# Kernel tuning notes

Measured on AMD Instinct MI355X. Metric: run time of the kernel, lower is better.

Reference implementation:

```python
import jax, jax.numpy as jnp
import numpy as np

MAX_ITERS = 256  # matches init_kwargs max_iters


def setup_inputs() -> dict:
    key = jax.random.key(0)
    k1, k2 = jax.random.split(key)
    H = W = 4096
    # classic Mandelbrot viewing window
    c_real = jax.random.uniform(k1, (H, W), jnp.float32, -2.0, 0.5)
    c_imag = jax.random.uniform(k2, (H, W), jnp.float32, -1.25, 1.25)
    return {"c_real": c_real, "c_imag": c_imag}


def reference(c_real, c_imag):
    # z starts at c (NOT zero), as in the torch module
    zr0 = c_real
    zi0 = c_imag
    active0 = jnp.ones(c_real.shape, dtype=bool)
    counts0 = jnp.full(c_real.shape, float(MAX_ITERS), dtype=c_real.dtype)

    def body(step, state):
        zr, zi, active, counts = state
        escaped_now = active & (zr * zr + zi * zi >= 4.0)
        counts = jnp.where(escaped_now, step.astype(counts.dtype), counts)
        active = active & ~escaped_now
        # torch loop only updates z for step < max_iters
        do_update = active & (step < MAX_ITERS)
        next_real = zr * zr - zi * zi + c_real
        next_imag = 2.0 * zr * zi + c_imag
        zr = jnp.where(do_update, next_real, zr)
        zi = jnp.where(do_update, next_imag, zi)
        return (zr, zi, active, counts)

    _, _, _, counts = jax.lax.fori_loop(
        0, MAX_ITERS + 1, body, (zr0, zi0, active0, counts0)
    )
    return counts
```

## Files before the change

### kernel.cpp

```cpp
#include <hip/hip_runtime.h>


#define MAX_ITERS 256

__device__ __forceinline__ float mul32(float a, float b) {
    float d; asm("v_mul_f32 %0, %1, %2" : "=v"(d) : "v"(a), "v"(b)); return d;
}
__device__ __forceinline__ float add32(float a, float b) {
    float d; asm("v_add_f32 %0, %1, %2" : "=v"(d) : "v"(a), "v"(b)); return d;
}
__device__ __forceinline__ float fma32(float a, float b, float c) {
    float d; asm("v_fma_f32 %0, %1, %2, %3" : "=v"(d) : "v"(a), "v"(b), "v"(c)); return d;
}
__device__ __forceinline__ float fma32_negc(float a, float b, float c) {
    float d; asm("v_fma_f32 %0, %1, %2, -%3" : "=v"(d) : "v"(a), "v"(b), "v"(c)); return d;
}

__device__ __forceinline__ void iter_checks(float cr, float ci,
                                            float& zr, float& zi,
                                            float& act, float& cnt, int nchecks)
{
    #pragma unroll 8
    for (int s = 0; s < nchecks; ++s) {
        const float zi2 = mul32(zi, zi);
        const float mag = fma32(zr, zr, zi2);
        act = (mag < 4.0f) ? act : 0.0f;
        cnt = cnt + act;
        const float t   = fma32_negc(zr, zr, zi2);
        const float nr  = add32(t, cr);
        const float t2  = add32(zr, zr);
        zi = fma32(t2, zi, ci);
        zr = nr;
    }
}

__global__ void zero_ctrs(unsigned char* ws) {
    if (threadIdx.x < 64) *(unsigned*)(ws + (size_t)threadIdx.x * 64u) = 0u;
}

__global__ __launch_bounds__(256) void mandel_stage_a(
    const float* __restrict__ c_real, const float* __restrict__ c_imag,
    float* __restrict__ out, unsigned char* __restrict__ ws,
    unsigned seg_cap, int n)
{
    int i = blockIdx.x * blockDim.x + threadIdx.x;
    if (i >= n) return;
    const float cr = c_real[i];
    const float ci = c_imag[i];

    const float xq = cr - 0.25f;
    const float q  = xq * xq + ci * ci;
    const bool in_card = (q * (q + xq) - 0.25f * ci * ci) < -1e-3f;
    const float xb = cr + 1.0f;
    const bool in_bulb = (xb * xb + ci * ci) < (0.0625f - 1e-3f);
    const bool shortcut = in_card | in_bulb;

    float zr = cr, zi = ci, act = 1.0f, cnt = 0.0f;
    iter_checks(cr, ci, zr, zi, act, cnt, 16);

    const bool surv = (!shortcut) && (act != 0.0f);

    const unsigned long long m = __ballot(surv);
    if (m != 0ull) {
        const int lane = __builtin_amdgcn_mbcnt_hi(
            ~0u, __builtin_amdgcn_mbcnt_lo(~0u, 0));
        const int leader = (int)__ffsll((unsigned long long)m) - 1;
        const int seg = blockIdx.x & 63;
        unsigned* ctr = (unsigned*)(ws + (size_t)seg * 64u);
        unsigned base = 0u;
        if (lane == leader) base = atomicAdd(ctr, (unsigned)__popcll(m));
        base = (unsigned)__shfl((int)base, leader, 64);
        if (surv) {
            const unsigned rank = (unsigned)__popcll(m & ((1ull << lane) - 1ull));
            const unsigned slot = base + rank;
            if (slot < seg_cap) {
                float4* q1 = (float4*)(ws + 4096);
                int*    q2 = (int*)(ws + 4096 + (size_t)seg_cap * 64u * 16u);
                const size_t p = (size_t)seg * seg_cap + slot;
                q1[p] = make_float4(zr, zi, cr, ci);
                q2[p] = i;
                return;
            }
            iter_checks(cr, ci, zr, zi, act, cnt, 240);
            out[i] = cnt;
            return;
        }
    }
    out[i] = shortcut ? 256.0f : cnt;
}

__global__ __launch_bounds__(256) void mandel_stage_b(
    float* __restrict__ out, const unsigned char* __restrict__ ws,
    unsigned seg_cap, int blocks_per_seg)
{
    const int seg = (int)(blockIdx.x & 63u);
    const int grp = (int)(blockIdx.x >> 6);
    const unsigned cnt_s = *(const unsigned*)(ws + (size_t)seg * 64u);
    const unsigned nq = (cnt_s < seg_cap) ? cnt_s : seg_cap;
    const float4* q1 = (const float4*)(ws + 4096);
    const int*    q2 = (const int*)(ws + 4096 + (size_t)seg_cap * 64u * 16u);
    const unsigned stride = (unsigned)blocks_per_seg * 256u;
    for (unsigned j = (unsigned)grp * 256u + threadIdx.x; j < nq; j += stride) {
        const size_t p = (size_t)seg * seg_cap + j;
        const float4 rec = q1[p];
        const int idx = q2[p];
        float zr = rec.x, zi = rec.y;
        const float cr = rec.z, ci = rec.w;
        float act = 1.0f, cnt = 16.0f;
        iter_checks(cr, ci, zr, zi, act, cnt, 240);
        out[idx] = cnt;
    }
}

__global__ __launch_bounds__(256) void mandel_mono(
    const float* __restrict__ c_real, const float* __restrict__ c_imag,
    float* __restrict__ out, int n)
{
    int i = blockIdx.x * blockDim.x + threadIdx.x;
    if (i >= n) return;
    const float cr = c_real[i], ci = c_imag[i];
    float zr = cr, zi = ci, act = 1.0f, cnt = 0.0f;
    iter_checks(cr, ci, zr, zi, act, cnt, MAX_ITERS);
    out[i] = cnt;
}

extern "C" void kernel_launch(void* const* d_in, const int* in_sizes, int n_in,
                              void* d_out, int out_size, void* d_ws, size_t ws_size,
                              hipStream_t stream)
{
    const float* c_real = (const float*)d_in[0];
    const float* c_imag = (const float*)d_in[1];
    float* out = (float*)d_out;
    const int n = in_sizes[0];
    const int block = 256;
    const int gridA = (n + block - 1) / block;

    unsigned char* ws = (unsigned char*)d_ws;
    const size_t avail = (ws_size > 4096) ? (ws_size - 4096) : 0;
    unsigned seg_cap = (unsigned)(avail / (64u * 20u));

    if (seg_cap < 1024u) {
        mandel_mono<<<gridA, block, 0, stream>>>(c_real, c_imag, out, n);
        return;
    }

    zero_ctrs<<<1, 64, 0, stream>>>(ws);
    mandel_stage_a<<<gridA, block, 0, stream>>>(c_real, c_imag, out, ws,
                                                seg_cap, n);
    const int blocks_per_seg = 256;
    mandel_stage_b<<<64 * blocks_per_seg, block, 0, stream>>>(out, ws, seg_cap,
                                                              blocks_per_seg);
}
```

Measured before the change: 258.3 us.

## Process four points per thread with packed FP32 math in both stages

Each thread in both the filter and tail stages now iterates four Mandelbrot points at once, using v_pk_mul/fma/add_f32 inline asm so two points share each packed instruction. Stage A uses vectorized float4 loads and one atomic per wave covering all four ballots. Stage B splits each segment's queue into four strided quarters per thread and drops to 32 blocks per segment. This trades more registers and lower occupancy, plus intra-thread divergence where one of the four points runs all 240 iterations, for half the ALU instruction count.

```diff
diff --git a/kernel.cpp b/kernel.cpp
--- a/kernel.cpp
+++ b/kernel.cpp
@@ -2,6 +2,9 @@
 
 
 #define MAX_ITERS 256
+
+typedef __attribute__((ext_vector_type(2))) float f32x2;
+typedef __attribute__((ext_vector_type(4))) float f32x4;
 
 __device__ __forceinline__ float mul32(float a, float b) {
     float d; asm("v_mul_f32 %0, %1, %2" : "=v"(d) : "v"(a), "v"(b)); return d;
@@ -34,62 +37,148 @@
     }
 }
 
-__global__ void zero_ctrs(unsigned char* ws) {
-    if (threadIdx.x < 64) *(unsigned*)(ws + (size_t)threadIdx.x * 64u) = 0u;
-}
-
-__global__ __launch_bounds__(256) void mandel_stage_a(
-    const float* __restrict__ c_real, const float* __restrict__ c_imag,
-    float* __restrict__ out, unsigned char* __restrict__ ws,
-    unsigned seg_cap, int n)
-{
-    int i = blockIdx.x * blockDim.x + threadIdx.x;
-    if (i >= n) return;
-    const float cr = c_real[i];
-    const float ci = c_imag[i];
-
+__device__ __forceinline__ void zstep2(const f32x2 cr, const f32x2 ci,
+                                       f32x2& zr, f32x2& zi, f32x2& mag)
+{
+    f32x2 s, t, u;
+    asm("v_pk_mul_f32 %0, %5, %5\n\t"
+        "v_pk_fma_f32 %1, %4, %4, %0\n\t"
+        "v_pk_fma_f32 %2, %4, %4, %0 neg_lo:[0,0,1] neg_hi:[0,0,1]\n\t"
+        "v_pk_add_f32 %3, %4, %4\n\t"
+        "v_pk_add_f32 %4, %2, %6\n\t"
+        "v_pk_fma_f32 %5, %3, %5, %7"
+        : "=&v"(s), "=&v"(mag), "=&v"(t), "=&v"(u), "+v"(zr), "+v"(zi)
+        : "v"(cr), "v"(ci));
+}
+
+__device__ __forceinline__ void check4(
+    const f32x2 crA, const f32x2 ciA, f32x2& zrA, f32x2& ziA,
+    const f32x2 crB, const f32x2 ciB, f32x2& zrB, f32x2& ziB,
+    float& act0, float& act1, float& act2, float& act3,
+    float& cnt0, float& cnt1, float& cnt2, float& cnt3)
+{
+    f32x2 magA, magB;
+    zstep2(crA, ciA, zrA, ziA, magA);
+    zstep2(crB, ciB, zrB, ziB, magB);
+    act0 = (magA.x < 4.0f) ? act0 : 0.0f;  cnt0 += act0;
+    act1 = (magA.y < 4.0f) ? act1 : 0.0f;  cnt1 += act1;
+    act2 = (magB.x < 4.0f) ? act2 : 0.0f;  cnt2 += act2;
+    act3 = (magB.y < 4.0f) ? act3 : 0.0f;  cnt3 += act3;
+}
+
+__device__ __forceinline__ int lane_id() {
+    return __builtin_amdgcn_mbcnt_hi(~0u, __builtin_amdgcn_mbcnt_lo(~0u, 0));
+}
+
+__device__ __forceinline__ bool in_shortcut(float cr, float ci) {
     const float xq = cr - 0.25f;
     const float q  = xq * xq + ci * ci;
     const bool in_card = (q * (q + xq) - 0.25f * ci * ci) < -1e-3f;
     const float xb = cr + 1.0f;
     const bool in_bulb = (xb * xb + ci * ci) < (0.0625f - 1e-3f);
-    const bool shortcut = in_card | in_bulb;
-
-    float zr = cr, zi = ci, act = 1.0f, cnt = 0.0f;
-    iter_checks(cr, ci, zr, zi, act, cnt, 16);
-
-    const bool surv = (!shortcut) && (act != 0.0f);
-
-    const unsigned long long m = __ballot(surv);
-    if (m != 0ull) {
-        const int lane = __builtin_amdgcn_mbcnt_hi(
-            ~0u, __builtin_amdgcn_mbcnt_lo(~0u, 0));
-        const int leader = (int)__ffsll((unsigned long long)m) - 1;
+    return in_card | in_bulb;
+}
+
+__global__ void zero_ctrs(unsigned char* ws) {
+    if (threadIdx.x < 64)
+        *(unsigned*)(ws + (size_t)threadIdx.x * 64u) = 0u;
+}
+
+__global__ __launch_bounds__(256) void mandel_stage_a_q(
+    const float* __restrict__ c_real, const float* __restrict__ c_imag,
+    float* __restrict__ out, unsigned char* __restrict__ ws,
+    unsigned seg_cap, int n)
+{
+    const int tq = blockIdx.x * blockDim.x + threadIdx.x;
+    const int p0 = tq << 2;
+    if (p0 >= n) return;
+
+    if (p0 + 3 >= n) {
+        for (int j = 0; j < 4 && p0 + j < n; ++j) {
+            const float cr = c_real[p0 + j], ci = c_imag[p0 + j];
+            if (in_shortcut(cr, ci)) { out[p0 + j] = 256.0f; continue; }
+            float zr = cr, zi = ci, act = 1.0f, cnt = 0.0f;
+            iter_checks(cr, ci, zr, zi, act, cnt, MAX_ITERS);
+            out[p0 + j] = cnt;
+        }
+        return;
+    }
+
+    const f32x4 cr4 = *(const f32x4*)(c_real + p0);
+    const f32x4 ci4 = *(const f32x4*)(c_imag + p0);
+    const f32x2 crA = {cr4.x, cr4.y}, ciA = {ci4.x, ci4.y};
+    const f32x2 crB = {cr4.z, cr4.w}, ciB = {ci4.z, ci4.w};
+    const bool sc0 = in_shortcut(cr4.x, ci4.x);
+    const bool sc1 = in_shortcut(cr4.y, ci4.y);
+    const bool sc2 = in_shortcut(cr4.z, ci4.z);
+    const bool sc3 = in_shortcut(cr4.w, ci4.w);
+
+    f32x2 zrA = crA, ziA = ciA, zrB = crB, ziB = ciB;
+    float act0 = 1.0f, act1 = 1.0f, act2 = 1.0f, act3 = 1.0f;
+    float cnt0 = 0.0f, cnt1 = 0.0f, cnt2 = 0.0f, cnt3 = 0.0f;
+    #pragma unroll
+    for (int s = 0; s < 16; ++s)
+        check4(crA, ciA, zrA, ziA, crB, ciB, zrB, ziB,
+               act0, act1, act2, act3, cnt0, cnt1, cnt2, cnt3);
+
+    const bool sv0 = (!sc0) && (act0 != 0.0f);
+    const bool sv1 = (!sc1) && (act1 != 0.0f);
+    const bool sv2 = (!sc2) && (act2 != 0.0f);
+    const bool sv3 = (!sc3) && (act3 != 0.0f);
+
+    const unsigned long long m0 = __ballot(sv0);
+    const unsigned long long m1 = __ballot(sv1);
+    const unsigned long long m2 = __ballot(sv2);
+    const unsigned long long m3 = __ballot(sv3);
+    const unsigned long long any = m0 | m1 | m2 | m3;
+    if (any != 0ull) {
+        const int lane = lane_id();
+        const int leader = (int)__ffsll(any) - 1;
         const int seg = blockIdx.x & 63;
         unsigned* ctr = (unsigned*)(ws + (size_t)seg * 64u);
+        const unsigned c0 = (unsigned)__popcll(m0);
+        const unsigned c1 = (unsigned)__popcll(m1);
+        const unsigned c2 = (unsigned)__popcll(m2);
+        const unsigned c3 = (unsigned)__popcll(m3);
         unsigned base = 0u;
-        if (lane == leader) base = atomicAdd(ctr, (unsigned)__popcll(m));
+        if (lane == leader) base = atomicAdd(ctr, c0 + c1 + c2 + c3);
         base = (unsigned)__shfl((int)base, leader, 64);
-        if (surv) {
-            const unsigned rank = (unsigned)__popcll(m & ((1ull << lane) - 1ull));
-            const unsigned slot = base + rank;
+        float4* qf = (float4*)(ws + 4096);
+        int*    qi = (int*)(ws + 4096 + (size_t)seg_cap * 64u * 16u);
+        const unsigned long long below = (1ull << lane) - 1ull;
+        const size_t segbase = (size_t)seg * seg_cap;
+        const unsigned pre1 = c0, pre2 = c0 + c1, pre3 = c0 + c1 + c2;
+
+        float zrv[4] = {zrA.x, zrA.y, zrB.x, zrB.y};
+        float ziv[4] = {ziA.x, ziA.y, ziB.x, ziB.y};
+        float crv[4] = {cr4.x, cr4.y, cr4.z, cr4.w};
+        float civ[4] = {ci4.x, ci4.y, ci4.z, ci4.w};
+        float cnv[4] = {cnt0, cnt1, cnt2, cnt3};
+        const bool svv[4] = {sv0, sv1, sv2, sv3};
+        const unsigned prev[4] = {0u, pre1, pre2, pre3};
+        const unsigned long long mv[4] = {m0, m1, m2, m3};
+        #pragma unroll
+        for (int j = 0; j < 4; ++j) {
+            if (!svv[j]) continue;
+            const unsigned slot = base + prev[j] +
+                (unsigned)__popcll(mv[j] & below);
             if (slot < seg_cap) {
-                float4* q1 = (float4*)(ws + 4096);
-                int*    q2 = (int*)(ws + 4096 + (size_t)seg_cap * 64u * 16u);
-                const size_t p = (size_t)seg * seg_cap + slot;
-                q1[p] = make_float4(zr, zi, cr, ci);
-                q2[p] = i;
-                return;
+                qf[segbase + slot] = make_float4(zrv[j], ziv[j], crv[j], civ[j]);
+                qi[segbase + slot] = p0 + j;
+            } else {
+                float zrs = zrv[j], zis = ziv[j], as = 1.0f, cs = cnv[j];
+                iter_checks(crv[j], civ[j], zrs, zis, as, cs, 240);
+                out[p0 + j] = cs;
             }
-            iter_checks(cr, ci, zr, zi, act, cnt, 240);
-            out[i] = cnt;
-            return;
         }
     }
-    out[i] = shortcut ? 256.0f : cnt;
-}
-
-__global__ __launch_bounds__(256) void mandel_stage_b(
+    if (!sv0) out[p0 + 0] = sc0 ? 256.0f : cnt0;
+    if (!sv1) out[p0 + 1] = sc1 ? 256.0f : cnt1;
+    if (!sv2) out[p0 + 2] = sc2 ? 256.0f : cnt2;
+    if (!sv3) out[p0 + 3] = sc3 ? 256.0f : cnt3;
+}
+
+__global__ __launch_bounds__(256) void mandel_stage_b_q(
     float* __restrict__ out, const unsigned char* __restrict__ ws,
     unsigned seg_cap, int blocks_per_seg)
 {
@@ -97,18 +186,39 @@
     const int grp = (int)(blockIdx.x >> 6);
     const unsigned cnt_s = *(const unsigned*)(ws + (size_t)seg * 64u);
     const unsigned nq = (cnt_s < seg_cap) ? cnt_s : seg_cap;
-    const float4* q1 = (const float4*)(ws + 4096);
-    const int*    q2 = (const int*)(ws + 4096 + (size_t)seg_cap * 64u * 16u);
+    const unsigned q = (nq + 3u) >> 2;
     const unsigned stride = (unsigned)blocks_per_seg * 256u;
-    for (unsigned j = (unsigned)grp * 256u + threadIdx.x; j < nq; j += stride) {
-        const size_t p = (size_t)seg * seg_cap + j;
-        const float4 rec = q1[p];
-        const int idx = q2[p];
-        float zr = rec.x, zi = rec.y;
-        const float cr = rec.z, ci = rec.w;
-        float act = 1.0f, cnt = 16.0f;
-        iter_checks(cr, ci, zr, zi, act, cnt, 240);
-        out[idx] = cnt;
+    const float4* qf = (const float4*)(ws + 4096);
+    const int*    qi = (const int*)(ws + 4096 + (size_t)seg_cap * 64u * 16u);
+    const size_t segbase = (size_t)seg * seg_cap;
+
+    for (unsigned k = (unsigned)grp * 256u + threadIdx.x; k < q; k += stride) {
+        const unsigned i1 = k + q, i2 = k + 2u * q, i3 = k + 3u * q;
+        const bool v1 = (i1 < nq), v2 = (i2 < nq), v3 = (i3 < nq);
+        const float4 r0 = qf[segbase + k];
+        const float4 r1 = v1 ? qf[segbase + i1] : r0;
+        const float4 r2 = v2 ? qf[segbase + i2] : r0;
+        const float4 r3 = v3 ? qf[segbase + i3] : r0;
+        const int idx0 = qi[segbase + k];
+        const int idx1 = v1 ? qi[segbase + i1] : -1;
+        const int idx2 = v2 ? qi[segbase + i2] : -1;
+        const int idx3 = v3 ? qi[segbase + i3] : -1;
+
+        f32x2 zrA = {r0.x, r1.x}, ziA = {r0.y, r1.y};
+        f32x2 crA = {r0.z, r1.z}, ciA = {r0.w, r1.w};
+        f32x2 zrB = {r2.x, r3.x}, ziB = {r2.y, r3.y};
+        f32x2 crB = {r2.z, r3.z}, ciB = {r2.w, r3.w};
+        float act0 = 1.0f, act1 = v1 ? 1.0f : 0.0f;
+        float act2 = v2 ? 1.0f : 0.0f, act3 = v3 ? 1.0f : 0.0f;
+        float cnt0 = 16.0f, cnt1 = 16.0f, cnt2 = 16.0f, cnt3 = 16.0f;
+        #pragma unroll 8
+        for (int s = 0; s < 240; ++s)
+            check4(crA, ciA, zrA, ziA, crB, ciB, zrB, ziB,
+                   act0, act1, act2, act3, cnt0, cnt1, cnt2, cnt3);
+        out[idx0] = cnt0;
+        if (v1) out[idx1] = cnt1;
+        if (v2) out[idx2] = cnt2;
+        if (v3) out[idx3] = cnt3;
     }
 }
 
@@ -133,21 +243,23 @@
     float* out = (float*)d_out;
     const int n = in_sizes[0];
     const int block = 256;
-    const int gridA = (n + block - 1) / block;
 
     unsigned char* ws = (unsigned char*)d_ws;
     const size_t avail = (ws_size > 4096) ? (ws_size - 4096) : 0;
-    unsigned seg_cap = (unsigned)(avail / (64u * 20u));
-
-    if (seg_cap < 1024u) {
+    const unsigned seg_cap = (unsigned)(avail / (64u * 20u));
+
+    if (seg_cap < 8192u) {
+        const int gridA = (n + block - 1) / block;
         mandel_mono<<<gridA, block, 0, stream>>>(c_real, c_imag, out, n);
         return;
     }
 
     zero_ctrs<<<1, 64, 0, stream>>>(ws);
-    mandel_stage_a<<<gridA, block, 0, stream>>>(c_real, c_imag, out, ws,
-                                                seg_cap, n);
-    const int blocks_per_seg = 256;
-    mandel_stage_b<<<64 * blocks_per_seg, block, 0, stream>>>(out, ws, seg_cap,
-                                                              blocks_per_seg);
-}
+
+    const int nquads = (n + 3) / 4;
+    const int gridA = (nquads + block - 1) / block;
+    mandel_stage_a_q<<<gridA, block, 0, stream>>>(c_real, c_imag, out,
+                                                  ws, seg_cap, n);
+    const int bps = 32;
+    mandel_stage_b_q<<<64 * bps, block, 0, stream>>>(out, ws, seg_cap, bps);
+}
```

New measurement: 237.6 us. 1.09x faster.
